# Performance work log

Measured on AMD Instinct MI355X. Metric: run time of the kernel, lower is better.

## Reference

```python
import jax, jax.numpy as jnp
import numpy as np
import math

N_EMBD = 1024
N_HEAD = 16
BLOCK = 2048
SPARSITY = 0.25
B, T = 2, 2048


def _make_mask_logits(rng):
    # Replicates the patterned init in SparseMixtureAttention.__init__.
    S = BLOCK
    logits = np.empty((N_HEAD, S, S), dtype=np.float32)
    for h in range(N_HEAD):
        if h % 3 == 0:  # banded pattern (bandwidth 16)
            i = np.arange(S)
            band = (np.abs(i[:, None] - i[None, :]) <= 16)
            logits[h] = np.where(band, rng.standard_normal((S, S)) + 2.0,
                                 rng.standard_normal((S, S)) - 2.0)
        elif h % 3 == 1:  # strided pattern: every 4th column
            strided = (np.arange(S)[None, :] % 4 == 0)
            logits[h] = np.where(strided, rng.standard_normal((S, S)) + 2.0,
                                 rng.standard_normal((S, S)) - 2.0)
        else:  # random pattern with given sparsity
            rnd = rng.random((S, S)) < SPARSITY
            logits[h] = np.where(rnd, rng.standard_normal((S, S)) + 2.0,
                                 rng.standard_normal((S, S)) - 2.0)
    # keep the diagonal unmasked so no causal row is fully masked (avoids NaN rows)
    d = np.arange(S)
    logits[:, d, d] = np.abs(logits[:, d, d]) + 2.0
    return logits.astype(np.float32)


def setup_inputs() -> dict:
    key = jax.random.key(0)
    ks = jax.random.split(key, 5)
    rng = np.random.default_rng(0)
    return {
        "x": jax.random.normal(ks[0], (B, T, N_EMBD), dtype=jnp.float32),
        "mask_logits": jnp.asarray(_make_mask_logits(rng)),
        "W_attn": jax.random.normal(ks[1], (3 * N_EMBD, N_EMBD), dtype=jnp.float32) * 0.02,
        "b_attn": jnp.zeros((3 * N_EMBD,), dtype=jnp.float32),
        "W_proj": jax.random.normal(ks[2], (N_EMBD, N_EMBD), dtype=jnp.float32) * 0.02,
        "b_proj": jnp.zeros((N_EMBD,), dtype=jnp.float32),
    }


def reference(x, mask_logits, W_attn, b_attn, W_proj, b_proj):
    Bx, Tx, C = x.shape
    H = mask_logits.shape[0]
    D = C // H
    qkv = x @ W_attn.T + b_attn                       # [B,T,3C]
    q, k, v = jnp.split(qkv, 3, axis=-1)
    q = q.reshape(Bx, Tx, H, D)
    k = k.reshape(Bx, Tx, H, D)
    v = v.reshape(Bx, Tx, H, D)
    att = jnp.einsum('bthd,bshd->bhts', q, k) * (1.0 / math.sqrt(D))  # [B,H,T,T]
    # forward value of the STE mask equals the hard mask (probs - probs.detach() == 0)
    keep = jax.nn.sigmoid(mask_logits[:, :Tx, :Tx]) > 0.5             # [H,T,T]
    causal = jnp.tril(jnp.ones((Tx, Tx), dtype=bool))
    mask = causal[None, :, :] & keep                                  # [H,T,T]
    att = jnp.where(mask[None], att, -jnp.inf)
    att = jax.nn.softmax(att, axis=-1)
    y = jnp.einsum('bhts,bshd->bthd', att, v).reshape(Bx, Tx, C)
    return y @ W_proj.T + b_proj
```

## Files before the change

kernel.cpp:

```cpp
#include <hip/hip_runtime.h>
#include <hip/hip_bf16.h>
#include <stdint.h>

typedef unsigned short u16;
typedef unsigned int u32;
typedef unsigned long long u64;
typedef __attribute__((ext_vector_type(8))) short bf16x8;
typedef __attribute__((ext_vector_type(4))) float f32x4;

#define NB 2
#define NH 16
#define TT 2048
#define DD 64
#define CC 1024

__device__ __forceinline__ u16 bf16bits(float f) {
    __hip_bfloat16 h = __float2bfloat16(f);
    return __builtin_bit_cast(unsigned short, h);
}

__device__ __forceinline__ void gload_lds16(const void* g, void* l) {
    __builtin_amdgcn_global_load_lds(
        (const __attribute__((address_space(1))) void*)g,
        (__attribute__((address_space(3))) void*)l, 16, 0, 0);
}

__global__ __launch_bounds__(256) void cvt_kernel(const float* __restrict__ in,
                                                  u16* __restrict__ out, int n4) {
    int idx = blockIdx.x * blockDim.x + threadIdx.x;
    int stride = gridDim.x * blockDim.x;
    for (int i = idx; i < n4; i += stride) {
        float4 v = reinterpret_cast<const float4*>(in)[i];
        ushort4 o;
        o.x = bf16bits(v.x); o.y = bf16bits(v.y);
        o.z = bf16bits(v.z); o.w = bf16bits(v.w);
        reinterpret_cast<ushort4*>(out)[i] = o;
    }
}

__global__ __launch_bounds__(256) void mask_cvt(const float* __restrict__ ml,
                                                unsigned char* __restrict__ mb) {
    int wid = (blockIdx.x * blockDim.x + threadIdx.x) >> 6;
    int lane = threadIdx.x & 63;
    int nwaves = (gridDim.x * blockDim.x) >> 6;
    for (int row = wid; row < NH * TT; row += nwaves) {
        int i = row & (TT - 1);
        const float* src = ml + (size_t)row * TT;
        unsigned char* dst = mb + (size_t)row * (TT / 8);
        for (int c8 = lane; c8 * 8 <= i; c8 += 64) {
            const float4* p = reinterpret_cast<const float4*>(src + c8 * 8);
            float4 a = p[0];
            float4 b = p[1];
            unsigned v = 0;
            v |= (a.x > 0.f) ? 1u : 0u;
            v |= (a.y > 0.f) ? 2u : 0u;
            v |= (a.z > 0.f) ? 4u : 0u;
            v |= (a.w > 0.f) ? 8u : 0u;
            v |= (b.x > 0.f) ? 16u : 0u;
            v |= (b.y > 0.f) ? 32u : 0u;
            v |= (b.z > 0.f) ? 64u : 0u;
            v |= (b.w > 0.f) ? 128u : 0u;
            dst[c8] = (unsigned char)v;
        }
    }
}

template <int MODE>
__global__ __launch_bounds__(256) void gemm_bt(
    const u16* __restrict__ A, const u16* __restrict__ Bw,
    const float* __restrict__ bias,
    u16* __restrict__ Qb, u16* __restrict__ Kb, u16* __restrict__ Vtb,
    float* __restrict__ Cout, int Kdim) {
    const int bm = blockIdx.y * 128;
    const int bn = blockIdx.x * 128;
    const int tid = threadIdx.x;
    const int w = tid >> 6, lane = tid & 63;
    const int lrow = lane & 15, lgrp = lane >> 4;
    const int wr = (w >> 1) * 64, wc = (w & 1) * 64;

    __shared__ __align__(16) u16 ABs[2][128 * 64];
    u16* As = ABs[0];
    u16* Bs = ABs[1];

    f32x4 acc[4][4] = {};

    const int nkt = Kdim >> 6;
    for (int kt = 0; kt < nkt; ++kt) {
        const int k0 = kt << 6;
#pragma unroll
        for (int i = 0; i < 4; ++i) {
            int e = i * 2048 + tid * 8;
            int r = e >> 6, c = e & 63;
            gload_lds16(A + (size_t)(bm + r) * Kdim + k0 + c, (char*)As + i * 4096 + w * 1024);
            gload_lds16(Bw + (size_t)(bn + r) * Kdim + k0 + c, (char*)Bs + i * 4096 + w * 1024);
        }
        __syncthreads();
#pragma unroll
        for (int kk = 0; kk < 2; ++kk) {
            bf16x8 af[4], bfz[4];
#pragma unroll
            for (int i = 0; i < 4; ++i)
                af[i] = *reinterpret_cast<const bf16x8*>(&As[(wr + i * 16 + lrow) * 64 + kk * 32 + lgrp * 8]);
#pragma unroll
            for (int i = 0; i < 4; ++i)
                bfz[i] = *reinterpret_cast<const bf16x8*>(&Bs[(wc + i * 16 + lrow) * 64 + kk * 32 + lgrp * 8]);
#pragma unroll
            for (int mi = 0; mi < 4; ++mi)
#pragma unroll
                for (int ni = 0; ni < 4; ++ni)
                    acc[mi][ni] = __builtin_amdgcn_mfma_f32_16x16x32_bf16(af[mi], bfz[ni], acc[mi][ni], 0, 0, 0);
        }
        __syncthreads();
    }

    const int sec = (MODE == 0) ? (bn >> 10) : 1;

    if (MODE == 0 && sec == 2) {
        u16* Tl = &ABs[0][0];
#pragma unroll
        for (int ni = 0; ni < 4; ++ni) {
            int nl = wc + ni * 16 + lrow;
            float bv = bias[bn + nl];
#pragma unroll
            for (int mi = 0; mi < 4; ++mi) {
                int ml2 = wr + mi * 16 + lgrp * 4;
                u64 pk = 0;
#pragma unroll
                for (int j = 0; j < 4; ++j)
                    pk |= (u64)bf16bits(acc[mi][ni][j] + bv) << (16 * j);
                int byte = nl * 256 + ((ml2 * 2) ^ ((nl & 7) << 4));
                *reinterpret_cast<u64*>((char*)Tl + byte) = pk;
            }
        }
        __syncthreads();
        int r = tid >> 1, half = tid & 1;
        int h = ((bn & 1023) >> 6) + (r >> 6);
        int d = r & 63;
        int b = bm >> 11;
        u16* gdst = Vtb + (((size_t)b * NH + h) * DD + d) * TT + (bm & 2047) + half * 64;
#pragma unroll
        for (int c = 0; c < 8; ++c) {
            uint4 v = *reinterpret_cast<const uint4*>(
                (char*)Tl + r * 256 + ((half * 128 + c * 16) ^ ((r & 7) << 4)));
            *reinterpret_cast<uint4*>(gdst + c * 8) = v;
        }
        return;
    }

#pragma unroll
    for (int ni = 0; ni < 4; ++ni) {
        int n = bn + wc + ni * 16 + lrow;
        float bv = bias[n];
#pragma unroll
        for (int mi = 0; mi < 4; ++mi) {
#pragma unroll
            for (int j = 0; j < 4; ++j) {
                int m = bm + wr + mi * 16 + lgrp * 4 + j;
                float v = acc[mi][ni][j] + bv;
                if (MODE == 1) {
                    Cout[(size_t)m * 1024 + n] = v;
                } else {
                    int h = (n & 1023) >> 6;
                    int d = n & 63;
                    int b = m >> 11;
                    int t = m & 2047;
                    if (sec == 0) {
                        Qb[(((size_t)b * NH + h) * TT + t) * DD + d] =
                            bf16bits(v * (0.125f * 1.4426950408889634f));
                    } else {
                        Kb[(((size_t)b * NH + h) * TT + t) * DD + d] = bf16bits(v);
                    }
                }
            }
        }
    }
}

__global__ __launch_bounds__(256) void attn_kernel(
    const u16* __restrict__ Qb, const u16* __restrict__ Kb,
    const u16* __restrict__ Vtb, const unsigned char* __restrict__ mb,
    u16* __restrict__ att_out) {
    const int slot = blockIdx.x >> 4;
    const int h = blockIdx.x & 15;
    const int b = blockIdx.y;
    const int qt = (slot < 16) ? (31 - slot) : (slot - 16);
    const int tid = threadIdx.x;
    const int w = tid >> 6, lane = tid & 63;
    const int lrow = lane & 15, g = lane >> 4;

    __shared__ __align__(16) u16 Ks[2][64 * 64];
    __shared__ __align__(16) u16 Vts[2][64 * 64];
    __shared__ __align__(16) u16 Ps[4][16 * 64];

    const u16* kg_base = &Kb[((size_t)b * NH + h) * TT * DD];
    const u16* vg_base = &Vtb[((size_t)b * NH + h) * DD * TT];

    auto STAGE = [&](int bufi, int kt) {
#pragma unroll
        for (int i = 0; i < 2; ++i) {
            int e = i * 2048 + tid * 8;
            int r = e >> 6, c = e & 63;
            int cs = c ^ ((r & 7) << 3);
            gload_lds16(kg_base + (size_t)kt * 64 * DD + r * DD + cs,
                        (char*)Ks[bufi] + i * 4096 + w * 1024);
            gload_lds16(vg_base + kt * 64 + (size_t)r * TT + cs,
                        (char*)Vts[bufi] + i * 4096 + w * 1024);
        }
    };

    const int qrow_g = qt * 64 + w * 16 + lrow;
    const int rswz = (lrow & 7) << 4;

    bf16x8 qf[2];
#pragma unroll
    for (int kk = 0; kk < 2; ++kk)
        qf[kk] = *reinterpret_cast<const bf16x8*>(
            &Qb[(((size_t)b * NH + h) * TT + qrow_g) * DD + kk * 32 + g * 8]);

    f32x4 oacc[4] = {};
    float l_run = 0.f;

    const unsigned char* mrow_base = mb + ((size_t)h * TT + qrow_g) * (TT / 8);
    char* PsW = (char*)&Ps[w][0];

    STAGE(0, 0);
    __syncthreads();
    int buf = 0;

#pragma unroll 1
    for (int kt = 0; kt <= qt; ++kt) {
        u64 mw = *reinterpret_cast<const u64*>(mrow_base + kt * 8);
        if (kt < qt) STAGE(buf ^ 1, kt + 1);

        f32x4 s[4] = {};
        __builtin_amdgcn_s_setprio(1);
#pragma unroll
        for (int kk = 0; kk < 2; ++kk)
#pragma unroll
            for (int nt = 0; nt < 4; ++nt) {
                bf16x8 kf = *reinterpret_cast<const bf16x8*>(
                    (char*)Ks[buf] + (((nt * 16 + lrow) * 128 + (kk * 32 + g * 8) * 2) ^ rswz));
                s[nt] = __builtin_amdgcn_mfma_f32_16x16x32_bf16(kf, qf[kk], s[nt], 0, 0, 0);
            }
        __builtin_amdgcn_s_setprio(0);

        u64 mws = mw >> (g * 4);
        u32 mlo = (u32)mws, mhi = (u32)(mws >> 32);
        float rs = 0.f;
        if (kt == qt) {
#pragma unroll
            for (int nt = 0; nt < 4; ++nt)
#pragma unroll
                for (int j = 0; j < 4; ++j) {
                    int bi = nt * 16 + j;
                    bool keep = (((bi < 32 ? mlo : mhi) >> (bi & 31)) & 1) &&
                                (kt * 64 + nt * 16 + g * 4 + j <= qrow_g);
                    float p = keep ? exp2f(s[nt][j]) : 0.f;
                    rs += p;
                    s[nt][j] = p;
                }
        } else {
#pragma unroll
            for (int nt = 0; nt < 4; ++nt)
#pragma unroll
                for (int j = 0; j < 4; ++j) {
                    int bi = nt * 16 + j;
                    bool keep = ((bi < 32 ? mlo : mhi) >> (bi & 31)) & 1;
                    float p = keep ? exp2f(s[nt][j]) : 0.f;
                    rs += p;
                    s[nt][j] = p;
                }
        }
        rs += __shfl_xor(rs, 16);
        rs += __shfl_xor(rs, 32);
        l_run += rs;

#pragma unroll
        for (int nt = 0; nt < 4; ++nt)
#pragma unroll
            for (int t = 0; t < 2; ++t) {
                u32 pk = (u32)bf16bits(s[nt][2 * t]) |
                         ((u32)bf16bits(s[nt][2 * t + 1]) << 16);
                int byte = (lrow * 128 + (nt * 16 + g * 4 + 2 * t) * 2) ^ rswz;
                *reinterpret_cast<u32*>(PsW + byte) = pk;
            }

        __builtin_amdgcn_s_setprio(1);
#pragma unroll
        for (int kk = 0; kk < 2; ++kk) {
            bf16x8 pf = *reinterpret_cast<const bf16x8*>(
                PsW + ((lrow * 128 + (kk * 32 + g * 8) * 2) ^ rswz));
#pragma unroll
            for (int dt = 0; dt < 4; ++dt) {
                bf16x8 vf = *reinterpret_cast<const bf16x8*>(
                    (char*)Vts[buf] + (((dt * 16 + lrow) * 128 + (kk * 32 + g * 8) * 2) ^ rswz));
                oacc[dt] = __builtin_amdgcn_mfma_f32_16x16x32_bf16(pf, vf, oacc[dt], 0, 0, 0);
            }
        }
        __builtin_amdgcn_s_setprio(0);

        __syncthreads();
        buf ^= 1;
    }

    float lb[4];
#pragma unroll
    for (int j = 0; j < 4; ++j)
        lb[j] = __shfl(l_run, (lane & 48) + g * 4 + j);
#pragma unroll
    for (int dt = 0; dt < 4; ++dt)
#pragma unroll
        for (int j = 0; j < 4; ++j) {
            int t = qt * 64 + w * 16 + g * 4 + j;
            float o = oacc[dt][j] / lb[j];
            att_out[((size_t)b * TT + t) * CC + h * DD + dt * 16 + lrow] = bf16bits(o);
        }
}

extern "C" void kernel_launch(void* const* d_in, const int* in_sizes, int n_in,
                              void* d_out, int out_size, void* d_ws, size_t ws_size,
                              hipStream_t stream) {
    const float* x = (const float*)d_in[0];
    const float* mask_logits = (const float*)d_in[1];
    const float* W_attn = (const float*)d_in[2];
    const float* b_attn = (const float*)d_in[3];
    const float* W_proj = (const float*)d_in[4];
    const float* b_proj = (const float*)d_in[5];
    float* out = (float*)d_out;

    char* ws = (char*)d_ws;
    u16* xb  = (u16*)(ws + 0);
    u16* Wa  = (u16*)(ws + (8u << 20));
    u16* Wp  = (u16*)(ws + (14u << 20));
    u16* Qb  = (u16*)(ws + (16u << 20));
    u16* Kb  = (u16*)(ws + (24u << 20));
    u16* Vtb = (u16*)(ws + (32u << 20));
    u16* att = (u16*)(ws + (40u << 20));
    unsigned char* mbits = (unsigned char*)(ws + 0);

    cvt_kernel<<<2048, 256, 0, stream>>>(x, xb, NB * TT * CC / 4);
    cvt_kernel<<<2048, 256, 0, stream>>>(W_attn, Wa, 3 * CC * CC / 4);
    cvt_kernel<<<1024, 256, 0, stream>>>(W_proj, Wp, CC * CC / 4);

    gemm_bt<0><<<dim3(24, 32), 256, 0, stream>>>(xb, Wa, b_attn, Qb, Kb, Vtb, nullptr, CC);
    mask_cvt<<<1024, 256, 0, stream>>>(mask_logits, mbits);
    attn_kernel<<<dim3(512, 2), 256, 0, stream>>>(Qb, Kb, Vtb, mbits, att);
    gemm_bt<1><<<dim3(8, 32), 256, 0, stream>>>(att, Wp, b_proj, nullptr, nullptr, nullptr, out, CC);
}
```

Baseline: 173.6 us.

## Split long causal query tiles across two blocks and merge partial outputs

Query tiles 16–31, which walk the most key tiles under the causal mask, are now split into two blocks that each cover half of the key range. Each half writes its unnormalized bf16 output and its row sum to a workspace buffer. A new combine kernel adds the two halves and divides by the total sum. The aim is to shorten the longest blocks and balance work across CUs. The cost is one extra kernel launch, the extra partial-output traffic, and rounding the partial sums to bf16 before normalization.

```diff
diff --git a/kernel.cpp b/kernel.cpp
--- a/kernel.cpp
+++ b/kernel.cpp
@@ -17,6 +17,11 @@
 __device__ __forceinline__ u16 bf16bits(float f) {
     __hip_bfloat16 h = __float2bfloat16(f);
     return __builtin_bit_cast(unsigned short, h);
+}
+
+__device__ __forceinline__ float bf2f(u16 u) {
+    u32 x = (u32)u << 16;
+    return __builtin_bit_cast(float, x);
 }
 
 __device__ __forceinline__ void gload_lds16(const void* g, void* l) {
@@ -179,11 +184,26 @@
 __global__ __launch_bounds__(256) void attn_kernel(
     const u16* __restrict__ Qb, const u16* __restrict__ Kb,
     const u16* __restrict__ Vtb, const unsigned char* __restrict__ mb,
-    u16* __restrict__ att_out) {
-    const int slot = blockIdx.x >> 4;
-    const int h = blockIdx.x & 15;
-    const int b = blockIdx.y;
-    const int qt = (slot < 16) ? (31 - slot) : (slot - 16);
+    u16* __restrict__ att_out, u16* __restrict__ Opart,
+    float* __restrict__ lpart) {
+    const int bid = blockIdx.x;
+    const int seg = bid >> 5;
+    const int hb = bid & 31;
+    const int h = hb >> 1, b = hb & 1;
+    int qt, k0, k1, half = 0;
+    bool split;
+    if (seg < 16) {
+        qt = seg; k0 = 0; k1 = qt + 1; split = false;
+    } else {
+        int i = seg - 16;
+        qt = 16 + (i >> 1);
+        half = i & 1;
+        int n = qt + 1, h1 = (n + 1) >> 1;
+        k0 = half ? h1 : 0;
+        k1 = half ? n : h1;
+        split = true;
+    }
+
     const int tid = threadIdx.x;
     const int w = tid >> 6, lane = tid & 63;
     const int lrow = lane & 15, g = lane >> 4;
@@ -223,14 +243,14 @@
     const unsigned char* mrow_base = mb + ((size_t)h * TT + qrow_g) * (TT / 8);
     char* PsW = (char*)&Ps[w][0];
 
-    STAGE(0, 0);
+    STAGE(0, k0);
     __syncthreads();
     int buf = 0;
 
 #pragma unroll 1
-    for (int kt = 0; kt <= qt; ++kt) {
+    for (int kt = k0; kt < k1; ++kt) {
         u64 mw = *reinterpret_cast<const u64*>(mrow_base + kt * 8);
-        if (kt < qt) STAGE(buf ^ 1, kt + 1);
+        if (kt + 1 < k1) STAGE(buf ^ 1, kt + 1);
 
         f32x4 s[4] = {};
         __builtin_amdgcn_s_setprio(1);
@@ -303,18 +323,57 @@
         buf ^= 1;
     }
 
-    float lb[4];
-#pragma unroll
-    for (int j = 0; j < 4; ++j)
-        lb[j] = __shfl(l_run, (lane & 48) + g * 4 + j);
-#pragma unroll
-    for (int dt = 0; dt < 4; ++dt)
-#pragma unroll
-        for (int j = 0; j < 4; ++j) {
-            int t = qt * 64 + w * 16 + g * 4 + j;
-            float o = oacc[dt][j] / lb[j];
-            att_out[((size_t)b * TT + t) * CC + h * DD + dt * 16 + lrow] = bf16bits(o);
-        }
+    if (!split) {
+        float lb[4];
+#pragma unroll
+        for (int j = 0; j < 4; ++j)
+            lb[j] = __shfl(l_run, (lane & 48) + g * 4 + j);
+#pragma unroll
+        for (int dt = 0; dt < 4; ++dt)
+#pragma unroll
+            for (int j = 0; j < 4; ++j) {
+                int t = qt * 64 + w * 16 + g * 4 + j;
+                float o = oacc[dt][j] / lb[j];
+                att_out[((size_t)b * TT + t) * CC + h * DD + dt * 16 + lrow] = bf16bits(o);
+            }
+    } else {
+        const int slot = (hb * 16 + (qt - 16)) * 2 + half;
+        u16* Op = Opart + (size_t)slot * 4096;
+#pragma unroll
+        for (int dt = 0; dt < 4; ++dt)
+#pragma unroll
+            for (int j = 0; j < 4; ++j) {
+                int row = w * 16 + g * 4 + j;
+                Op[row * 64 + dt * 16 + lrow] = bf16bits(oacc[dt][j]);
+            }
+        if (g == 0) lpart[(size_t)slot * 64 + w * 16 + lrow] = l_run;
+    }
+}
+
+__global__ __launch_bounds__(256) void combine_kernel(
+    const u16* __restrict__ Opart, const float* __restrict__ lpart,
+    u16* __restrict__ att_out) {
+    const int cid = blockIdx.x;
+    const int hb = cid >> 4;
+    const int h = hb >> 1, b = hb & 1;
+    const int qt = 16 + (cid & 15);
+    const int t = threadIdx.x;
+    const int row = t >> 2, c0 = (t & 3) << 4;
+
+    const u16* p0 = Opart + ((size_t)cid * 2) * 4096 + row * 64 + c0;
+    const u16* p1 = p0 + 4096;
+    float l = lpart[(size_t)cid * 128 + row] + lpart[(size_t)cid * 128 + 64 + row];
+    float inv = 1.0f / l;
+
+    u16 ov[16];
+#pragma unroll
+    for (int i = 0; i < 16; ++i)
+        ov[i] = bf16bits((bf2f(p0[i]) + bf2f(p1[i])) * inv);
+
+    u16* dst = att_out + ((size_t)b * TT + qt * 64 + row) * CC + h * DD + c0;
+#pragma unroll
+    for (int i = 0; i < 2; ++i)
+        reinterpret_cast<uint4*>(dst)[i] = reinterpret_cast<const uint4*>(ov)[i];
 }
 
 extern "C" void kernel_launch(void* const* d_in, const int* in_sizes, int n_in,
@@ -329,13 +388,15 @@
     float* out = (float*)d_out;
 
     char* ws = (char*)d_ws;
-    u16* xb  = (u16*)(ws + 0);
-    u16* Wa  = (u16*)(ws + (8u << 20));
-    u16* Wp  = (u16*)(ws + (14u << 20));
-    u16* Qb  = (u16*)(ws + (16u << 20));
-    u16* Kb  = (u16*)(ws + (24u << 20));
-    u16* Vtb = (u16*)(ws + (32u << 20));
-    u16* att = (u16*)(ws + (40u << 20));
+    u16* xb    = (u16*)(ws + 0);
+    u16* Wa    = (u16*)(ws + (8u << 20));
+    u16* Qb    = (u16*)(ws + (16u << 20));
+    u16* Kb    = (u16*)(ws + (24u << 20));
+    u16* Vtb   = (u16*)(ws + (32u << 20));
+    u16* att   = (u16*)(ws + (40u << 20));
+    u16* Wp    = (u16*)(ws + (48u << 20));
+    float* lpart = (float*)(ws + (50u << 20));
+    u16* Opart = (u16*)(ws + (8u << 20));
     unsigned char* mbits = (unsigned char*)(ws + 0);
 
     cvt_kernel<<<2048, 256, 0, stream>>>(x, xb, NB * TT * CC / 4);
@@ -344,6 +405,7 @@
 
     gemm_bt<0><<<dim3(24, 32), 256, 0, stream>>>(xb, Wa, b_attn, Qb, Kb, Vtb, nullptr, CC);
     mask_cvt<<<1024, 256, 0, stream>>>(mask_logits, mbits);
-    attn_kernel<<<dim3(512, 2), 256, 0, stream>>>(Qb, Kb, Vtb, mbits, att);
+    attn_kernel<<<1536, 256, 0, stream>>>(Qb, Kb, Vtb, mbits, att, Opart, lpart);
+    combine_kernel<<<512, 256, 0, stream>>>(Opart, lpart, att);
     gemm_bt<1><<<dim3(8, 32), 256, 0, stream>>>(att, Wp, b_proj, nullptr, nullptr, nullptr, out, CC);
 }
```

Result: no change. 175.3 us (+1.0%).

## Fuse input conversions and mask packing into one prep kernel; relax attention barriers

Applied to the files above, without the earlier changes.

The three fp32-to-bf16 conversion kernels and the mask bit-packing kernel are merged into one launch. The mask is moved to its own workspace region so it can run before the QKV GEMM without conflicting with xb, and mask rows are paired i and 2047-i for load balance. In the attention loop, __syncthreads is replaced by explicit vmcnt waits plus raw s_barrier so the prefetch of the next tile can stay in flight while the current tile is consumed. This cuts launch count and synchronisation overhead, but relies on hand-counted vmcnt values matching the STAGE load count.

```diff
diff --git a/kernel.cpp b/kernel.cpp
--- a/kernel.cpp
+++ b/kernel.cpp
@@ -25,42 +25,52 @@
         (__attribute__((address_space(3))) void*)l, 16, 0, 0);
 }
 
-__global__ __launch_bounds__(256) void cvt_kernel(const float* __restrict__ in,
-                                                  u16* __restrict__ out, int n4) {
-    int idx = blockIdx.x * blockDim.x + threadIdx.x;
-    int stride = gridDim.x * blockDim.x;
-    for (int i = idx; i < n4; i += stride) {
-        float4 v = reinterpret_cast<const float4*>(in)[i];
-        ushort4 o;
-        o.x = bf16bits(v.x); o.y = bf16bits(v.y);
-        o.z = bf16bits(v.z); o.w = bf16bits(v.w);
-        reinterpret_cast<ushort4*>(out)[i] = o;
-    }
-}
-
-__global__ __launch_bounds__(256) void mask_cvt(const float* __restrict__ ml,
-                                                unsigned char* __restrict__ mb) {
-    int wid = (blockIdx.x * blockDim.x + threadIdx.x) >> 6;
-    int lane = threadIdx.x & 63;
-    int nwaves = (gridDim.x * blockDim.x) >> 6;
-    for (int row = wid; row < NH * TT; row += nwaves) {
-        int i = row & (TT - 1);
-        const float* src = ml + (size_t)row * TT;
-        unsigned char* dst = mb + (size_t)row * (TT / 8);
-        for (int c8 = lane; c8 * 8 <= i; c8 += 64) {
-            const float4* p = reinterpret_cast<const float4*>(src + c8 * 8);
-            float4 a = p[0];
-            float4 b = p[1];
-            unsigned v = 0;
-            v |= (a.x > 0.f) ? 1u : 0u;
-            v |= (a.y > 0.f) ? 2u : 0u;
-            v |= (a.z > 0.f) ? 4u : 0u;
-            v |= (a.w > 0.f) ? 8u : 0u;
-            v |= (b.x > 0.f) ? 16u : 0u;
-            v |= (b.y > 0.f) ? 32u : 0u;
-            v |= (b.z > 0.f) ? 64u : 0u;
-            v |= (b.w > 0.f) ? 128u : 0u;
-            dst[c8] = (unsigned char)v;
+__global__ __launch_bounds__(256) void prep_all(
+    const float* __restrict__ x, const float* __restrict__ Wa_f,
+    const float* __restrict__ Wp_f, const float* __restrict__ ml,
+    u16* __restrict__ xb, u16* __restrict__ wab, u16* __restrict__ wpb,
+    unsigned char* __restrict__ mb) {
+    const int bid = blockIdx.x;
+    if (bid < 512) {
+        int idx = bid * 256 + threadIdx.x;
+        for (int i = idx; i < 2097152; i += 512 * 256) {
+            const float* src; u16* dst; int off;
+            if (i < 1048576)      { src = x;    dst = xb;  off = i; }
+            else if (i < 1835008) { src = Wa_f; dst = wab; off = i - 1048576; }
+            else                  { src = Wp_f; dst = wpb; off = i - 1835008; }
+            float4 v = reinterpret_cast<const float4*>(src)[off];
+            ushort4 o;
+            o.x = bf16bits(v.x); o.y = bf16bits(v.y);
+            o.z = bf16bits(v.z); o.w = bf16bits(v.w);
+            reinterpret_cast<ushort4*>(dst)[off] = o;
+        }
+    } else {
+        const int wid = ((bid - 512) << 2) + (threadIdx.x >> 6);
+        const int lane = threadIdx.x & 63;
+        const int i0 = wid & 2047;
+        const int hbase = (wid >> 11) << 3;
+#pragma unroll 1
+        for (int k = 0; k < 8; ++k) {
+            int h = hbase + k;
+            int i = (k & 1) ? (2047 - i0) : i0;
+            int row = h * 2048 + i;
+            const float* src = ml + (size_t)row * TT;
+            unsigned char* dst = mb + (size_t)row * (TT / 8);
+            for (int c8 = lane; c8 * 8 <= i; c8 += 64) {
+                const float4* p = reinterpret_cast<const float4*>(src + c8 * 8);
+                float4 a = p[0];
+                float4 b = p[1];
+                unsigned v = 0;
+                v |= (a.x > 0.f) ? 1u : 0u;
+                v |= (a.y > 0.f) ? 2u : 0u;
+                v |= (a.z > 0.f) ? 4u : 0u;
+                v |= (a.w > 0.f) ? 8u : 0u;
+                v |= (b.x > 0.f) ? 16u : 0u;
+                v |= (b.y > 0.f) ? 32u : 0u;
+                v |= (b.z > 0.f) ? 64u : 0u;
+                v |= (b.w > 0.f) ? 128u : 0u;
+                dst[c8] = (unsigned char)v;
+            }
         }
     }
 }
@@ -224,13 +234,19 @@
     char* PsW = (char*)&Ps[w][0];
 
     STAGE(0, 0);
-    __syncthreads();
     int buf = 0;
 
 #pragma unroll 1
     for (int kt = 0; kt <= qt; ++kt) {
         u64 mw = *reinterpret_cast<const u64*>(mrow_base + kt * 8);
-        if (kt < qt) STAGE(buf ^ 1, kt + 1);
+        if (kt < qt) {
+            STAGE(buf ^ 1, kt + 1);
+            asm volatile("s_waitcnt vmcnt(5)" ::: "memory");
+        } else {
+            asm volatile("s_waitcnt vmcnt(1)" ::: "memory");
+        }
+        __builtin_amdgcn_sched_barrier(0);
+        asm volatile("s_barrier" ::: "memory");
 
         f32x4 s[4] = {};
         __builtin_amdgcn_s_setprio(1);
@@ -299,7 +315,7 @@
         }
         __builtin_amdgcn_s_setprio(0);
 
-        __syncthreads();
+        asm volatile("s_barrier" ::: "memory");
         buf ^= 1;
     }
 
@@ -336,14 +352,11 @@
     u16* Kb  = (u16*)(ws + (24u << 20));
     u16* Vtb = (u16*)(ws + (32u << 20));
     u16* att = (u16*)(ws + (40u << 20));
-    unsigned char* mbits = (unsigned char*)(ws + 0);
-
-    cvt_kernel<<<2048, 256, 0, stream>>>(x, xb, NB * TT * CC / 4);
-    cvt_kernel<<<2048, 256, 0, stream>>>(W_attn, Wa, 3 * CC * CC / 4);
-    cvt_kernel<<<1024, 256, 0, stream>>>(W_proj, Wp, CC * CC / 4);
-
+    unsigned char* mbits = (unsigned char*)(ws + (48u << 20));
+
+    prep_all<<<1536, 256, 0, stream>>>(x, W_attn, W_proj, mask_logits,
+                                       xb, Wa, Wp, mbits);
     gemm_bt<0><<<dim3(24, 32), 256, 0, stream>>>(xb, Wa, b_attn, Qb, Kb, Vtb, nullptr, CC);
-    mask_cvt<<<1024, 256, 0, stream>>>(mask_logits, mbits);
     attn_kernel<<<dim3(512, 2), 256, 0, stream>>>(Qb, Kb, Vtb, mbits, att);
     gemm_bt<1><<<dim3(8, 32), 256, 0, stream>>>(att, Wp, b_proj, nullptr, nullptr, nullptr, out, CC);
 }
```

Result: faster. 165.6 us (-4.6%).
